# Performance work log

Measured on AMD Instinct MI355X. Metric: run time of the kernel, lower is better.

The kernel has to match this reference:

```python
import jax, jax.numpy as jnp
import numpy as np

B, H, W, C = 16, 32, 32, 512
L, CT = 77, 512
NH, HD = 8, 64
G = 32          # GroupNorm groups
EPS = 1e-6      # flax GroupNorm default epsilon
NEG = -1e10


def group_norm(x, scale, bias):
    # flax GroupNorm on [b, n, c]: stats over (n, channels-within-group) per (b, group)
    b, n, c = x.shape
    xg = x.reshape(b, n, G, c // G)
    mu = xg.mean(axis=(1, 3), keepdims=True)
    var = xg.var(axis=(1, 3), keepdims=True)
    xg = (xg - mu) * jax.lax.rsqrt(var + EPS)
    return xg.reshape(b, n, c) * scale + bias


def setup_inputs() -> dict:
    key = jax.random.key(0)
    ks = jax.random.split(key, 8)
    w = lambda k, shape: jax.random.normal(k, shape, jnp.float32) * 0.02
    return {
        "inputs": jax.random.normal(ks[0], (B, H, W, C), jnp.float32),
        "text_enc": jax.random.normal(ks[1], (B, L, CT), jnp.float32),
        "text_mask": jnp.ones((B, L), jnp.int32),
        "gn_q_scale": jnp.ones((C,), jnp.float32),
        "gn_q_bias": jnp.zeros((C,), jnp.float32),
        "gn_kv_scale": jnp.ones((C,), jnp.float32),
        "gn_kv_bias": jnp.zeros((C,), jnp.float32),
        "gn_t_scale": jnp.ones((CT,), jnp.float32),
        "gn_t_bias": jnp.zeros((CT,), jnp.float32),
        "Wq": w(ks[2], (C, NH, HD)),
        "Wk_self": w(ks[3], (C, NH, HD)),
        "Wv_self": w(ks[4], (C, NH, HD)),
        "Wk_cross": w(ks[5], (CT, NH, HD)),
        "Wv_cross": w(ks[6], (CT, NH, HD)),
        "Wout": w(ks[7], (NH, HD, C)),
    }


def reference(inputs, text_enc, text_mask,
              gn_q_scale, gn_q_bias, gn_kv_scale, gn_kv_bias,
              gn_t_scale, gn_t_bias,
              Wq, Wk_self, Wv_self, Wk_cross, Wv_cross, Wout):
    b, h, w, c = inputs.shape
    n = h * w
    x = inputs.reshape(b, n, c)

    x_q = group_norm(x, gn_q_scale, gn_q_bias)
    x_kv = group_norm(x, gn_kv_scale, gn_kv_bias)
    t = group_norm(text_enc, gn_t_scale, gn_t_bias)

    # q/k/v projections; fused: KV = concat(self-KV from image, cross-KV from text)
    scale = jnp.asarray(1.0 / np.sqrt(HD), inputs.dtype)
    q = jnp.einsum('bqc,chd->bqhd', x_q, Wq) * scale  # scale_attn_logits
    k = jnp.concatenate([jnp.einsum('bkc,chd->bkhd', x_kv, Wk_self),
                         jnp.einsum('blc,chd->blhd', t, Wk_cross)], axis=1)
    v = jnp.concatenate([jnp.einsum('bkc,chd->bkhd', x_kv, Wv_self),
                         jnp.einsum('blc,chd->blhd', t, Wv_cross)], axis=1)

    # make_attention_mask(ones[b,n], concat(ones[b,n], text_mask)) -> [b,1,n,n+l];
    # query mask is all ones so only the KV mask matters.
    kv_mask = jnp.concatenate(
        [jnp.ones((b, n), jnp.bool_), text_mask > 0], axis=1)  # [b, n+l]

    logits = jnp.einsum('bqhd,bkhd->bhqk', q, k)  # [b, nh, n, n+l]
    logits = jnp.where(kv_mask[:, None, None, :], logits, jnp.asarray(NEG, logits.dtype))
    probs = jax.nn.softmax(logits, axis=-1)
    attn = jnp.einsum('bhqk,bkhd->bqhd', probs, v)
    out = jnp.einsum('bqhd,hdc->bqc', attn, Wout)
    return out.reshape(b, h, w, c) + inputs
```

## Files before the change

kernel.cpp:

```cpp
#include <hip/hip_runtime.h>
#include <hip/hip_bf16.h>

typedef __hip_bfloat16 bf16;
typedef __attribute__((ext_vector_type(4))) short short4v;
typedef __attribute__((ext_vector_type(8))) short short8;
typedef __attribute__((ext_vector_type(4))) float f32x4;
typedef __attribute__((ext_vector_type(16))) float f32x16;
#define MFMA16(a, b, c) __builtin_amdgcn_mfma_f32_16x16x32_bf16(a, b, c, 0, 0, 0)
#define MFMA32(a, b, c) __builtin_amdgcn_mfma_f32_32x32x16_bf16(a, b, c, 0, 0, 0)

#define BB   16
#define CCH  512
#define NN   1024
#define LLT  77
#define LPAD 128
#define NHH  8
#define HDD  64
#define GGN  32
#define NKV  1101
#define KVP  1152

__device__ __forceinline__ unsigned short f2bu(float f){
  bf16 h = __float2bfloat16(f);
  return *reinterpret_cast<unsigned short*>(&h);
}

__device__ __forceinline__ unsigned pk2(float lo, float hi){
  __hip_bfloat162 h = __float22bfloat162_rn(make_float2(lo, hi));
  return *reinterpret_cast<unsigned*>(&h);
}

__device__ __forceinline__ void pl32swap(unsigned &a, unsigned &b){
  asm("v_permlane32_swap_b32 %0, %1" : "+v"(a), "+v"(b));
}

__global__ __launch_bounds__(256) void gn_stats_kernel(
    const float* __restrict__ ximg, const float* __restrict__ xtxt,
    float* __restrict__ stats )
{
  int isimg = blockIdx.x < 512;
  int bid = blockIdx.x & 511;
  int b = bid >> 5, g = bid & 31;
  int npos = isimg ? NN : LLT;
  const float* xb = (isimg ? ximg : xtxt) + (size_t)b * npos * CCH + g * 16;
  int tot4 = npos * 4;
  float s = 0.f, s2 = 0.f;
  for (int e = threadIdx.x; e < tot4; e += 256){
    int n = e >> 2, cq = (e & 3) * 4;
    float4 v = *(const float4*)(xb + (size_t)n * CCH + cq);
    s  += v.x + v.y + v.z + v.w;
    s2 += v.x * v.x + v.y * v.y + v.z * v.z + v.w * v.w;
  }
  __shared__ float sh1[256], sh2[256];
  sh1[threadIdx.x] = s; sh2[threadIdx.x] = s2;
  __syncthreads();
  for (int off = 128; off > 0; off >>= 1){
    if (threadIdx.x < off){
      sh1[threadIdx.x] += sh1[threadIdx.x + off];
      sh2[threadIdx.x] += sh2[threadIdx.x + off];
    }
    __syncthreads();
  }
  if (threadIdx.x == 0){
    float inv = 1.f / (float)(npos * 16);
    float m = sh1[0] * inv;
    float var = sh2[0] * inv - m * m;
    float* mu = stats + (isimg ? 0 : 1024);
    mu[bid] = m;
    mu[512 + bid] = rsqrtf(var + 1e-6f);
  }
}

__global__ __launch_bounds__(256) void prep_weights_kernel(
    const float* __restrict__ W0, const float* __restrict__ W1,
    const float* __restrict__ W2, const float* __restrict__ W3,
    const float* __restrict__ W4, const float* __restrict__ W5,
    bf16* __restrict__ Wt)
{
  int wsel = blockIdx.z;
  const float* W = wsel == 0 ? W0 : wsel == 1 ? W1 : wsel == 2 ? W2 :
                   wsel == 3 ? W3 : wsel == 4 ? W4 : W5;
  bf16* dst = Wt + (size_t)wsel * CCH * CCH;
  int n0 = blockIdx.x * 64, k0 = blockIdx.y * 64;

  __shared__ alignas(16) float Ws[64][68];
  int r = threadIdx.x >> 2, c = (threadIdx.x & 3) * 16;
  const float* src = W + (size_t)(k0 + r) * CCH + n0 + c;
  *(float4*)&Ws[r][c]      = *(const float4*)(src);
  *(float4*)&Ws[r][c + 4]  = *(const float4*)(src + 4);
  *(float4*)&Ws[r][c + 8]  = *(const float4*)(src + 8);
  *(float4*)&Ws[r][c + 12] = *(const float4*)(src + 12);
  __syncthreads();

  int nr = threadIdx.x >> 2, kc = (threadIdx.x & 3) * 16;
  union { uint4 v[2]; unsigned short s[16]; } o;
  #pragma unroll
  for (int j = 0; j < 16; j++) o.s[j] = f2bu(Ws[kc + j][nr]);
  bf16* d = dst + (size_t)(n0 + nr) * CCH + k0 + kc;
  *(uint4*)d = o.v[0];
  *(uint4*)(d + 8) = o.v[1];
}

__global__ __launch_bounds__(256) void norm_all_kernel(
    const float* __restrict__ x, const float* __restrict__ t,
    const float* __restrict__ stats,
    const float* __restrict__ gqs, const float* __restrict__ gqb,
    const float* __restrict__ gks, const float* __restrict__ gkb,
    const float* __restrict__ gts, const float* __restrict__ gtb,
    bf16* __restrict__ Xq, bf16* __restrict__ Xkv, bf16* __restrict__ Tn)
{
  if (blockIdx.x < 4096){
    size_t e = ((size_t)blockIdx.x * 256 + threadIdx.x) * 8;
    int b  = (int)(e >> 19);
    int ch = (int)(e & 511);
    int g  = ch >> 4;
    float m = stats[b * GGN + g], r = stats[512 + b * GGN + g];
    float4 x0 = *(const float4*)(x + e);
    float4 x1 = *(const float4*)(x + e + 4);
    float4 sq0 = *(const float4*)(gqs + ch), sq1 = *(const float4*)(gqs + ch + 4);
    float4 bq0 = *(const float4*)(gqb + ch), bq1 = *(const float4*)(gqb + ch + 4);
    float4 sk0 = *(const float4*)(gks + ch), sk1 = *(const float4*)(gks + ch + 4);
    float4 bk0 = *(const float4*)(gkb + ch), bk1 = *(const float4*)(gkb + ch + 4);
    float xs[8] = {x0.x,x0.y,x0.z,x0.w,x1.x,x1.y,x1.z,x1.w};
    float sqv[8] = {sq0.x,sq0.y,sq0.z,sq0.w,sq1.x,sq1.y,sq1.z,sq1.w};
    float bqv[8] = {bq0.x,bq0.y,bq0.z,bq0.w,bq1.x,bq1.y,bq1.z,bq1.w};
    float skv[8] = {sk0.x,sk0.y,sk0.z,sk0.w,sk1.x,sk1.y,sk1.z,sk1.w};
    float bkv[8] = {bk0.x,bk0.y,bk0.z,bk0.w,bk1.x,bk1.y,bk1.z,bk1.w};
    union { uint4 v; unsigned short s[8]; } oq, ok;
    #pragma unroll
    for (int j = 0; j < 8; j++){
      float nx = (xs[j] - m) * r;
      oq.s[j] = f2bu((nx * sqv[j] + bqv[j]) * 0.18033688f);
      ok.s[j] = f2bu(nx * skv[j] + bkv[j]);
    }
    *(uint4*)(Xq + e)  = oq.v;
    *(uint4*)(Xkv + e) = ok.v;
  } else {
    size_t e = ((size_t)(blockIdx.x - 4096) * 256 + threadIdx.x) * 8;
    int b  = (int)(e >> 16);
    int rem = (int)(e & 65535);
    int l  = rem >> 9;
    int ch = rem & 511;
    union { uint4 v; unsigned short s[8]; } o;
    if (l < LLT){
      int g = ch >> 4;
      float m = stats[1024 + b * GGN + g], r = stats[1536 + b * GGN + g];
      const float* src = t + ((size_t)b * LLT + l) * CCH + ch;
      float4 x0 = *(const float4*)src, x1 = *(const float4*)(src + 4);
      float4 s0 = *(const float4*)(gts + ch), s1 = *(const float4*)(gts + ch + 4);
      float4 b0 = *(const float4*)(gtb + ch), b1 = *(const float4*)(gtb + ch + 4);
      float xs[8] = {x0.x,x0.y,x0.z,x0.w,x1.x,x1.y,x1.z,x1.w};
      float sv[8] = {s0.x,s0.y,s0.z,s0.w,s1.x,s1.y,s1.z,s1.w};
      float bv[8] = {b0.x,b0.y,b0.z,b0.w,b1.x,b1.y,b1.z,b1.w};
      #pragma unroll
      for (int j = 0; j < 8; j++) o.s[j] = f2bu((xs[j] - m) * r * sv[j] + bv[j]);
    } else {
      o.v = make_uint4(0, 0, 0, 0);
    }
    *(uint4*)(Tn + e) = o.v;
  }
}

__global__ __launch_bounds__(256) void proj_self_mfma(
    const bf16* __restrict__ Xq, const bf16* __restrict__ Xkv,
    const bf16* __restrict__ Wt,
    bf16* __restrict__ Qo, bf16* __restrict__ Ko, bf16* __restrict__ Vo)
{
  const int tid  = threadIdx.x;
  const int wave = tid >> 6, lane = tid & 63;
  const int l16 = lane & 15, quad = lane >> 4;
  const int h  = blockIdx.x;
  const int n0 = blockIdx.y * 64;
  const int b  = blockIdx.z;

  __shared__ bf16 Aq[64][72], Ak[64][72];
  __shared__ bf16 Bq[64][72], Bk[64][72], Bv[64][72];

  const bf16* Wq  = Wt;
  const bf16* Wks = Wt + 1 * CCH * CCH;
  const bf16* Wvs = Wt + 2 * CCH * CCH;

  f32x4 sq[4], sk[4], sv[4];
  #pragma unroll
  for (int nt = 0; nt < 4; nt++){
    sq[nt] = (f32x4){0.f,0.f,0.f,0.f};
    sk[nt] = (f32x4){0.f,0.f,0.f,0.f};
    sv[nt] = (f32x4){0.f,0.f,0.f,0.f};
  }

  const int sr = tid >> 2, sc = (tid & 3) * 16;
  const bf16* p_aq = Xq  + ((size_t)b * NN + n0 + sr) * CCH + sc;
  const bf16* p_ak = Xkv + ((size_t)b * NN + n0 + sr) * CCH + sc;
  const bf16* p_bq = Wq  + (size_t)(h * 64 + sr) * CCH + sc;
  const bf16* p_bk = Wks + (size_t)(h * 64 + sr) * CCH + sc;
  const bf16* p_bv = Wvs + (size_t)(h * 64 + sr) * CCH + sc;

  uint4 raq0 = *(const uint4*)p_aq,       raq1 = *(const uint4*)(p_aq + 8);
  uint4 rak0 = *(const uint4*)p_ak,       rak1 = *(const uint4*)(p_ak + 8);
  uint4 rbq0 = *(const uint4*)p_bq,       rbq1 = *(const uint4*)(p_bq + 8);
  uint4 rbk0 = *(const uint4*)p_bk,       rbk1 = *(const uint4*)(p_bk + 8);
  uint4 rbv0 = *(const uint4*)p_bv,       rbv1 = *(const uint4*)(p_bv + 8);

  for (int kt = 0; kt < 8; kt++){
    *(uint4*)&Aq[sr][sc]     = raq0;  *(uint4*)&Aq[sr][sc + 8] = raq1;
    *(uint4*)&Ak[sr][sc]     = rak0;  *(uint4*)&Ak[sr][sc + 8] = rak1;
    *(uint4*)&Bq[sr][sc]     = rbq0;  *(uint4*)&Bq[sr][sc + 8] = rbq1;
    *(uint4*)&Bk[sr][sc]     = rbk0;  *(uint4*)&Bk[sr][sc + 8] = rbk1;
    *(uint4*)&Bv[sr][sc]     = rbv0;  *(uint4*)&Bv[sr][sc + 8] = rbv1;
    if (kt < 7){
      const int k1 = (kt + 1) * 64;
      raq0 = *(const uint4*)(p_aq + k1);  raq1 = *(const uint4*)(p_aq + k1 + 8);
      rak0 = *(const uint4*)(p_ak + k1);  rak1 = *(const uint4*)(p_ak + k1 + 8);
      rbq0 = *(const uint4*)(p_bq + k1);  rbq1 = *(const uint4*)(p_bq + k1 + 8);
      rbk0 = *(const uint4*)(p_bk + k1);  rbk1 = *(const uint4*)(p_bk + k1 + 8);
      rbv0 = *(const uint4*)(p_bv + k1);  rbv1 = *(const uint4*)(p_bv + k1 + 8);
    }
    __syncthreads();

    const short8 aq0 = *(const short8*)&Aq[wave * 16 + l16][quad * 8];
    const short8 aq1 = *(const short8*)&Aq[wave * 16 + l16][32 + quad * 8];
    const short8 ak0 = *(const short8*)&Ak[wave * 16 + l16][quad * 8];
    const short8 ak1 = *(const short8*)&Ak[wave * 16 + l16][32 + quad * 8];

    #pragma unroll
    for (int nt = 0; nt < 4; nt++){
      const short8 bq0 = *(const short8*)&Bq[nt * 16 + l16][quad * 8];
      const short8 bq1 = *(const short8*)&Bq[nt * 16 + l16][32 + quad * 8];
      sq[nt] = MFMA16(aq0, bq0, sq[nt]);
      sq[nt] = MFMA16(aq1, bq1, sq[nt]);
      const short8 bk0 = *(const short8*)&Bk[nt * 16 + l16][quad * 8];
      const short8 bk1 = *(const short8*)&Bk[nt * 16 + l16][32 + quad * 8];
      sk[nt] = MFMA16(ak0, bk0, sk[nt]);
      sk[nt] = MFMA16(ak1, bk1, sk[nt]);
      const short8 bv0 = *(const short8*)&Bv[nt * 16 + l16][quad * 8];
      const short8 bv1 = *(const short8*)&Bv[nt * 16 + l16][32 + quad * 8];
      sv[nt] = MFMA16(ak0, bv0, sv[nt]);
      sv[nt] = MFMA16(ak1, bv1, sv[nt]);
    }
    __syncthreads();
  }

  #pragma unroll
  for (int r = 0; r < 4; r++){
    int n = n0 + wave * 16 + quad * 4 + r;
    bf16* qd = Qo + (((size_t)b * NHH + h) * NN + n) * HDD + l16;
    bf16* kd = Ko + (((size_t)b * NHH + h) * KVP + n) * HDD + l16;
    #pragma unroll
    for (int nt = 0; nt < 4; nt++){
      qd[nt * 16] = __float2bfloat16(sq[nt][r]);
      kd[nt * 16] = __float2bfloat16(sk[nt][r]);
    }
  }

  __syncthreads();
  #pragma unroll
  for (int nt = 0; nt < 4; nt++)
    #pragma unroll
    for (int r = 0; r < 4; r++)
      Bq[nt * 16 + l16][wave * 16 + quad * 4 + r] = __float2bfloat16(sv[nt][r]);
  __syncthreads();
  {
    int d = tid >> 2, c = (tid & 3) * 16;
    bf16* vd = Vo + (((size_t)b * NHH + h) * HDD + d) * KVP + n0 + c;
    *(uint4*)vd       = *(const uint4*)&Bq[d][c];
    *(uint4*)(vd + 8) = *(const uint4*)&Bq[d][c + 8];
  }
}

__global__ __launch_bounds__(256) void proj_cross_mfma(
    const bf16* __restrict__ Tn, const bf16* __restrict__ Wt,
    bf16* __restrict__ Ko, bf16* __restrict__ Vo)
{
  const int tid  = threadIdx.x;
  const int wave = tid >> 6, lane = tid & 63;
  const int l16 = lane & 15, quad = lane >> 4;
  const int h  = blockIdx.x;
  const int l0 = blockIdx.y * 64;
  const int b  = blockIdx.z;

  __shared__ bf16 At[64][72];
  __shared__ bf16 Bk[64][72], Bv[64][72];

  const bf16* Wkc = Wt + 3 * CCH * CCH;
  const bf16* Wvc = Wt + 4 * CCH * CCH;

  f32x4 sk[4], sv[4];
  #pragma unroll
  for (int nt = 0; nt < 4; nt++){
    sk[nt] = (f32x4){0.f,0.f,0.f,0.f};
    sv[nt] = (f32x4){0.f,0.f,0.f,0.f};
  }

  const int sr = tid >> 2, sc = (tid & 3) * 16;
  const bf16* p_a  = Tn  + ((size_t)b * LPAD + l0 + sr) * CCH + sc;
  const bf16* p_bk = Wkc + (size_t)(h * 64 + sr) * CCH + sc;
  const bf16* p_bv = Wvc + (size_t)(h * 64 + sr) * CCH + sc;

  uint4 ra0 = *(const uint4*)p_a,   ra1 = *(const uint4*)(p_a + 8);
  uint4 rk0 = *(const uint4*)p_bk,  rk1 = *(const uint4*)(p_bk + 8);
  uint4 rv0 = *(const uint4*)p_bv,  rv1 = *(const uint4*)(p_bv + 8);

  for (int kt = 0; kt < 8; kt++){
    *(uint4*)&At[sr][sc]     = ra0;  *(uint4*)&At[sr][sc + 8] = ra1;
    *(uint4*)&Bk[sr][sc]     = rk0;  *(uint4*)&Bk[sr][sc + 8] = rk1;
    *(uint4*)&Bv[sr][sc]     = rv0;  *(uint4*)&Bv[sr][sc + 8] = rv1;
    if (kt < 7){
      const int k1 = (kt + 1) * 64;
      ra0 = *(const uint4*)(p_a + k1);   ra1 = *(const uint4*)(p_a + k1 + 8);
      rk0 = *(const uint4*)(p_bk + k1);  rk1 = *(const uint4*)(p_bk + k1 + 8);
      rv0 = *(const uint4*)(p_bv + k1);  rv1 = *(const uint4*)(p_bv + k1 + 8);
    }
    __syncthreads();

    const short8 a0 = *(const short8*)&At[wave * 16 + l16][quad * 8];
    const short8 a1 = *(const short8*)&At[wave * 16 + l16][32 + quad * 8];
    #pragma unroll
    for (int nt = 0; nt < 4; nt++){
      const short8 bk0 = *(const short8*)&Bk[nt * 16 + l16][quad * 8];
      const short8 bk1 = *(const short8*)&Bk[nt * 16 + l16][32 + quad * 8];
      sk[nt] = MFMA16(a0, bk0, sk[nt]);
      sk[nt] = MFMA16(a1, bk1, sk[nt]);
      const short8 bv0 = *(const short8*)&Bv[nt * 16 + l16][quad * 8];
      const short8 bv1 = *(const short8*)&Bv[nt * 16 + l16][32 + quad * 8];
      sv[nt] = MFMA16(a0, bv0, sv[nt]);
      sv[nt] = MFMA16(a1, bv1, sv[nt]);
    }
    __syncthreads();
  }

  #pragma unroll
  for (int r = 0; r < 4; r++){
    int kvrow = NN + l0 + wave * 16 + quad * 4 + r;
    bf16* kd = Ko + (((size_t)b * NHH + h) * KVP + kvrow) * HDD + l16;
    #pragma unroll
    for (int nt = 0; nt < 4; nt++)
      kd[nt * 16] = __float2bfloat16(sk[nt][r]);
  }

  __syncthreads();
  #pragma unroll
  for (int nt = 0; nt < 4; nt++)
    #pragma unroll
    for (int r = 0; r < 4; r++)
      Bk[nt * 16 + l16][wave * 16 + quad * 4 + r] = __float2bfloat16(sv[nt][r]);
  __syncthreads();
  {
    int d = tid >> 2, c = (tid & 3) * 16;
    bf16* vd = Vo + (((size_t)b * NHH + h) * HDD + d) * KVP + NN + l0 + c;
    *(uint4*)vd       = *(const uint4*)&Bk[d][c];
    *(uint4*)(vd + 8) = *(const uint4*)&Bk[d][c + 8];
  }
}

__global__ __launch_bounds__(256, 4) void attn_mfma_kernel(
    const bf16* __restrict__ Q, const bf16* __restrict__ K,
    const bf16* __restrict__ Vt, const int* __restrict__ tmask,
    bf16* __restrict__ Ao)
{
  const int tid  = threadIdx.x;
  const int wave = tid >> 6;
  const int lane = tid & 63;
  const int l31  = lane & 31;
  const int hi   = lane >> 5;
  const int q0 = blockIdx.x * 128;
  const int h  = blockIdx.y;
  const int b  = blockIdx.z;

  __shared__ alignas(16) bf16 KV[2][2][64][72];

  const bf16* qp = Q + (((size_t)b * NHH + h) * NN + q0 + wave * 32 + l31) * HDD + hi * 8;
  short8 qf[4];
  qf[0] = *(const short8*)(qp);
  qf[1] = *(const short8*)(qp + 16);
  qf[2] = *(const short8*)(qp + 32);
  qf[3] = *(const short8*)(qp + 48);

  f32x16 o_acc[2];
  #pragma unroll
  for (int dt = 0; dt < 2; dt++)
    #pragma unroll
    for (int i = 0; i < 16; i++) o_acc[dt][i] = 0.f;
  float lrow = 0.f;

  const size_t kbase = ((size_t)b * NHH + h) * KVP;
  const size_t vbase = ((size_t)b * NHH + h) * (size_t)HDD * KVP;

  const int sr = tid >> 2;
  const int sc = (tid & 3) * 16;
  const bf16* kp = K  + (kbase + sr) * HDD + sc;
  const bf16* vp = Vt + vbase + (size_t)sr * KVP + sc;

  uint4 kr0 = *(const uint4*)kp, kr1 = *(const uint4*)(kp + 8);
  uint4 vr0 = *(const uint4*)vp, vr1 = *(const uint4*)(vp + 8);
  *(uint4*)&KV[0][0][sr][sc]     = kr0;
  *(uint4*)&KV[0][0][sr][sc + 8] = kr1;
  *(uint4*)&KV[0][1][sr][sc]     = vr0;
  *(uint4*)&KV[0][1][sr][sc + 8] = vr1;
  kr0 = *(const uint4*)(kp + 4096); kr1 = *(const uint4*)(kp + 4096 + 8);
  vr0 = *(const uint4*)(vp + 64);   vr1 = *(const uint4*)(vp + 64 + 8);
  __syncthreads();

  for (int kt = 0; kt < 18; kt++){
    const int cur = kt & 1;
    if (kt + 1 < 18){
      *(uint4*)&KV[cur ^ 1][0][sr][sc]     = kr0;
      *(uint4*)&KV[cur ^ 1][0][sr][sc + 8] = kr1;
      *(uint4*)&KV[cur ^ 1][1][sr][sc]     = vr0;
      *(uint4*)&KV[cur ^ 1][1][sr][sc + 8] = vr1;
    }
    if (kt + 2 < 18){
      const size_t ko = (size_t)(kt + 2) * 4096;
      const int    vo = (kt + 2) * 64;
      kr0 = *(const uint4*)(kp + ko); kr1 = *(const uint4*)(kp + ko + 8);
      vr0 = *(const uint4*)(vp + vo); vr1 = *(const uint4*)(vp + vo + 8);
    }

    const bf16 (*Ks)[72] = KV[cur][0];
    const bf16 (*Vs)[72] = KV[cur][1];
    const int kv0 = kt * 64;

    #pragma unroll
    for (int t = 0; t < 2; t++){
      f32x16 s;
      #pragma unroll
      for (int i = 0; i < 16; i++) s[i] = 0.f;
      const short8 kf0 = *(const short8*)&Ks[t * 32 + l31][hi * 8];
      const short8 kf1 = *(const short8*)&Ks[t * 32 + l31][16 + hi * 8];
      const short8 kf2 = *(const short8*)&Ks[t * 32 + l31][32 + hi * 8];
      const short8 kf3 = *(const short8*)&Ks[t * 32 + l31][48 + hi * 8];
      s = MFMA32(kf0, qf[0], s);
      s = MFMA32(kf1, qf[1], s);
      s = MFMA32(kf2, qf[2], s);
      s = MFMA32(kf3, qf[3], s);

      if (kv0 + 64 > NN){
        #pragma unroll
        for (int r = 0; r < 16; r++){
          int idx = kv0 - NN + t * 32 + (r & 3) + 8 * (r >> 2) + 4 * hi;
          int ci = idx < LLT ? idx : LLT - 1;
          float rep = (idx < LLT)
                        ? (tmask[b * LLT + ci] > 0 ? 1e30f : -1e10f)
                        : -1e30f;
          s[r] = fminf(s[r], rep);
        }
      }

      #pragma unroll
      for (int r = 0; r < 16; r++){
        s[r] = exp2f(s[r]);
        lrow += s[r];
      }

      unsigned w0 = pk2(s[0],  s[1]),  w1 = pk2(s[2],  s[3]);
      unsigned w2 = pk2(s[4],  s[5]),  w3 = pk2(s[6],  s[7]);
      unsigned w4 = pk2(s[8],  s[9]),  w5 = pk2(s[10], s[11]);
      unsigned w6 = pk2(s[12], s[13]), w7 = pk2(s[14], s[15]);
      pl32swap(w0, w2);
      pl32swap(w1, w3);
      pl32swap(w4, w6);
      pl32swap(w5, w7);
      union { unsigned u[4]; short8 s8; } pf0, pf1;
      pf0.u[0] = w0; pf0.u[1] = w1; pf0.u[2] = w2; pf0.u[3] = w3;
      pf1.u[0] = w4; pf1.u[1] = w5; pf1.u[2] = w6; pf1.u[3] = w7;

      #pragma unroll
      for (int dt = 0; dt < 2; dt++){
        const short8 vf0 = *(const short8*)&Vs[dt * 32 + l31][t * 32 + hi * 8];
        const short8 vf1 = *(const short8*)&Vs[dt * 32 + l31][t * 32 + 16 + hi * 8];
        o_acc[dt] = MFMA32(pf0.s8, vf0, o_acc[dt]);
        o_acc[dt] = MFMA32(pf1.s8, vf1, o_acc[dt]);
      }
    }
    __syncthreads();
  }

  lrow += __shfl_xor(lrow, 32);
  #pragma unroll
  for (int r = 0; r < 16; r++){
    const int ql = (r & 3) + 8 * (r >> 2) + 4 * hi;
    float linv = 1.f / __shfl(lrow, ql);
    const int n = q0 + wave * 32 + ql;
    bf16* dst = Ao + ((size_t)b * NN + n) * CCH + h * HDD + l31;
    dst[0]  = __float2bfloat16(o_acc[0][r] * linv);
    dst[32] = __float2bfloat16(o_acc[1][r] * linv);
  }
}

__global__ __launch_bounds__(256) void outproj_mfma(
    const bf16* __restrict__ A, const bf16* __restrict__ Wt,
    const float* __restrict__ resid, float* __restrict__ out)
{
  const int tid  = threadIdx.x;
  const int wave = tid >> 6, lane = tid & 63;
  const int l16 = lane & 15, quad = lane >> 4;
  const int col0 = blockIdx.x * 64;
  const int n0   = blockIdx.y * 64;
  const int b    = blockIdx.z;

  __shared__ bf16 As[64][72], Bs[64][72];
  const bf16* Wo = Wt + 5 * CCH * CCH;

  f32x4 o[4];
  #pragma unroll
  for (int nt = 0; nt < 4; nt++) o[nt] = (f32x4){0.f,0.f,0.f,0.f};

  const int sr = tid >> 2, sc = (tid & 3) * 16;
  const bf16* p_a = A  + ((size_t)b * NN + n0 + sr) * CCH + sc;
  const bf16* p_b = Wo + (size_t)(col0 + sr) * CCH + sc;

  uint4 ra0 = *(const uint4*)p_a,  ra1 = *(const uint4*)(p_a + 8);
  uint4 rb0 = *(const uint4*)p_b,  rb1 = *(const uint4*)(p_b + 8);

  for (int kt = 0; kt < 8; kt++){
    *(uint4*)&As[sr][sc]     = ra0;  *(uint4*)&As[sr][sc + 8] = ra1;
    *(uint4*)&Bs[sr][sc]     = rb0;  *(uint4*)&Bs[sr][sc + 8] = rb1;
    if (kt < 7){
      const int k1 = (kt + 1) * 64;
      ra0 = *(const uint4*)(p_a + k1);  ra1 = *(const uint4*)(p_a + k1 + 8);
      rb0 = *(const uint4*)(p_b + k1);  rb1 = *(const uint4*)(p_b + k1 + 8);
    }
    __syncthreads();

    const short8 a0 = *(const short8*)&As[wave * 16 + l16][quad * 8];
    const short8 a1 = *(const short8*)&As[wave * 16 + l16][32 + quad * 8];
    #pragma unroll
    for (int nt = 0; nt < 4; nt++){
      const short8 b0 = *(const short8*)&Bs[nt * 16 + l16][quad * 8];
      const short8 b1 = *(const short8*)&Bs[nt * 16 + l16][32 + quad * 8];
      o[nt] = MFMA16(a0, b0, o[nt]);
      o[nt] = MFMA16(a1, b1, o[nt]);
    }
    __syncthreads();
  }

  #pragma unroll
  for (int r = 0; r < 4; r++){
    size_t row = (size_t)b * NN + n0 + wave * 16 + quad * 4 + r;
    #pragma unroll
    for (int nt = 0; nt < 4; nt++){
      int col = col0 + nt * 16 + l16;
      out[row * CCH + col] = o[nt][r] + resid[row * CCH + col];
    }
  }
}

extern "C" void kernel_launch(void* const* d_in, const int* in_sizes, int n_in,
                              void* d_out, int out_size, void* d_ws, size_t ws_size,
                              hipStream_t stream)
{
  const float* x     = (const float*)d_in[0];
  const float* txt   = (const float*)d_in[1];
  const int*   tmask = (const int*)d_in[2];
  const float* gqs   = (const float*)d_in[3];
  const float* gqb   = (const float*)d_in[4];
  const float* gks   = (const float*)d_in[5];
  const float* gkb   = (const float*)d_in[6];
  const float* gts   = (const float*)d_in[7];
  const float* gtb   = (const float*)d_in[8];
  const float* Wq    = (const float*)d_in[9];
  const float* Wks   = (const float*)d_in[10];
  const float* Wvs   = (const float*)d_in[11];
  const float* Wkc   = (const float*)d_in[12];
  const float* Wvc   = (const float*)d_in[13];
  const float* Wout  = (const float*)d_in[14];

  float* stats = (float*)d_ws;
  bf16* WtAll = (bf16*)(stats + 2048);
  bf16* Xq  = WtAll + (size_t)6 * CCH * CCH;
  bf16* Xkv = Xq  + (size_t)BB * NN * CCH;
  bf16* Tn  = Xkv + (size_t)BB * NN * CCH;
  bf16* Qw  = Tn  + (size_t)BB * LPAD * CCH;
  bf16* Kw  = Qw  + (size_t)BB * NHH * NN * HDD;
  bf16* Vw  = Kw  + (size_t)BB * NHH * KVP * HDD;
  bf16* Aw  = Xq;

  gn_stats_kernel<<<1024, 256, 0, stream>>>(x, txt, stats);
  prep_weights_kernel<<<dim3(8, 8, 6), 256, 0, stream>>>(
      Wq, Wks, Wvs, Wkc, Wvc, Wout, WtAll);
  norm_all_kernel<<<4608, 256, 0, stream>>>(
      x, txt, stats, gqs, gqb, gks, gkb, gts, gtb, Xq, Xkv, Tn);
  proj_self_mfma<<<dim3(8, 16, BB), 256, 0, stream>>>(
      Xq, Xkv, WtAll, Qw, Kw, Vw);
  proj_cross_mfma<<<dim3(8, 2, BB), 256, 0, stream>>>(
      Tn, WtAll, Kw, Vw);
  attn_mfma_kernel<<<dim3(8, NHH, BB), 256, 0, stream>>>(Qw, Kw, Vw, tmask, Aw);
  outproj_mfma<<<dim3(8, 16, BB), 256, 0, stream>>>(Aw, WtAll, x, (float*)d_out);
}
```

Baseline: 288.9 us.

## Use 128x128 block tiles for projection GEMMs and MFMA row-sum in attention

```diff
diff --git a/kernel.cpp b/kernel.cpp
--- a/kernel.cpp
+++ b/kernel.cpp
@@ -2,7 +2,6 @@
 #include <hip/hip_bf16.h>
 
 typedef __hip_bfloat16 bf16;
-typedef __attribute__((ext_vector_type(4))) short short4v;
 typedef __attribute__((ext_vector_type(8))) short short8;
 typedef __attribute__((ext_vector_type(4))) float f32x4;
 typedef __attribute__((ext_vector_type(16))) float f32x16;
@@ -169,101 +168,106 @@
   const int tid  = threadIdx.x;
   const int wave = tid >> 6, lane = tid & 63;
   const int l16 = lane & 15, quad = lane >> 4;
-  const int h  = blockIdx.x;
-  const int n0 = blockIdx.y * 64;
-  const int b  = blockIdx.z;
-
-  __shared__ bf16 Aq[64][72], Ak[64][72];
-  __shared__ bf16 Bq[64][72], Bk[64][72], Bv[64][72];
-
-  const bf16* Wq  = Wt;
-  const bf16* Wks = Wt + 1 * CCH * CCH;
-  const bf16* Wvs = Wt + 2 * CCH * CCH;
-
-  f32x4 sq[4], sk[4], sv[4];
-  #pragma unroll
-  for (int nt = 0; nt < 4; nt++){
-    sq[nt] = (f32x4){0.f,0.f,0.f,0.f};
-    sk[nt] = (f32x4){0.f,0.f,0.f,0.f};
-    sv[nt] = (f32x4){0.f,0.f,0.f,0.f};
-  }
+  const int wr = wave >> 1, wc = wave & 1;
+  const int ct = blockIdx.x;
+  const int rt = blockIdx.y;
+  const int mat = ct >> 2;
+  const int cm0 = (ct & 3) * 128;
+  const int b  = rt >> 3;
+  const int n0 = (rt & 7) * 128;
+
+  __shared__ bf16 T[4][64][72];
+
+  const bf16* A  = (mat == 0) ? Xq : Xkv;
+  const bf16* Bw = Wt + (size_t)mat * CCH * CCH + (size_t)cm0 * CCH;
+
+  f32x4 acc[4][4];
+  #pragma unroll
+  for (int rf = 0; rf < 4; rf++)
+    #pragma unroll
+    for (int cf = 0; cf < 4; cf++) acc[rf][cf] = (f32x4){0.f,0.f,0.f,0.f};
 
   const int sr = tid >> 2, sc = (tid & 3) * 16;
-  const bf16* p_aq = Xq  + ((size_t)b * NN + n0 + sr) * CCH + sc;
-  const bf16* p_ak = Xkv + ((size_t)b * NN + n0 + sr) * CCH + sc;
-  const bf16* p_bq = Wq  + (size_t)(h * 64 + sr) * CCH + sc;
-  const bf16* p_bk = Wks + (size_t)(h * 64 + sr) * CCH + sc;
-  const bf16* p_bv = Wvs + (size_t)(h * 64 + sr) * CCH + sc;
-
-  uint4 raq0 = *(const uint4*)p_aq,       raq1 = *(const uint4*)(p_aq + 8);
-  uint4 rak0 = *(const uint4*)p_ak,       rak1 = *(const uint4*)(p_ak + 8);
-  uint4 rbq0 = *(const uint4*)p_bq,       rbq1 = *(const uint4*)(p_bq + 8);
-  uint4 rbk0 = *(const uint4*)p_bk,       rbk1 = *(const uint4*)(p_bk + 8);
-  uint4 rbv0 = *(const uint4*)p_bv,       rbv1 = *(const uint4*)(p_bv + 8);
+  const bf16* pa0 = A  + ((size_t)b * NN + n0 + sr) * CCH + sc;
+  const bf16* pa1 = pa0 + (size_t)64 * CCH;
+  const bf16* pb0 = Bw + (size_t)sr * CCH + sc;
+  const bf16* pb1 = pb0 + (size_t)64 * CCH;
+
+  uint4 rA0a = *(const uint4*)pa0, rA0b = *(const uint4*)(pa0 + 8);
+  uint4 rA1a = *(const uint4*)pa1, rA1b = *(const uint4*)(pa1 + 8);
+  uint4 rB0a = *(const uint4*)pb0, rB0b = *(const uint4*)(pb0 + 8);
+  uint4 rB1a = *(const uint4*)pb1, rB1b = *(const uint4*)(pb1 + 8);
 
   for (int kt = 0; kt < 8; kt++){
-    *(uint4*)&Aq[sr][sc]     = raq0;  *(uint4*)&Aq[sr][sc + 8] = raq1;
-    *(uint4*)&Ak[sr][sc]     = rak0;  *(uint4*)&Ak[sr][sc + 8] = rak1;
-    *(uint4*)&Bq[sr][sc]     = rbq0;  *(uint4*)&Bq[sr][sc + 8] = rbq1;
-    *(uint4*)&Bk[sr][sc]     = rbk0;  *(uint4*)&Bk[sr][sc + 8] = rbk1;
-    *(uint4*)&Bv[sr][sc]     = rbv0;  *(uint4*)&Bv[sr][sc + 8] = rbv1;
+    *(uint4*)&T[0][sr][sc] = rA0a;  *(uint4*)&T[0][sr][sc + 8] = rA0b;
+    *(uint4*)&T[1][sr][sc] = rA1a;  *(uint4*)&T[1][sr][sc + 8] = rA1b;
+    *(uint4*)&T[2][sr][sc] = rB0a;  *(uint4*)&T[2][sr][sc + 8] = rB0b;
+    *(uint4*)&T[3][sr][sc] = rB1a;  *(uint4*)&T[3][sr][sc + 8] = rB1b;
     if (kt < 7){
       const int k1 = (kt + 1) * 64;
-      raq0 = *(const uint4*)(p_aq + k1);  raq1 = *(const uint4*)(p_aq + k1 + 8);
-      rak0 = *(const uint4*)(p_ak + k1);  rak1 = *(const uint4*)(p_ak + k1 + 8);
-      rbq0 = *(const uint4*)(p_bq + k1);  rbq1 = *(const uint4*)(p_bq + k1 + 8);
-      rbk0 = *(const uint4*)(p_bk + k1);  rbk1 = *(const uint4*)(p_bk + k1 + 8);
-      rbv0 = *(const uint4*)(p_bv + k1);  rbv1 = *(const uint4*)(p_bv + k1 + 8);
-    }
-    __syncthreads();
-
-    const short8 aq0 = *(const short8*)&Aq[wave * 16 + l16][quad * 8];
-    const short8 aq1 = *(const short8*)&Aq[wave * 16 + l16][32 + quad * 8];
-    const short8 ak0 = *(const short8*)&Ak[wave * 16 + l16][quad * 8];
-    const short8 ak1 = *(const short8*)&Ak[wave * 16 + l16][32 + quad * 8];
-
-    #pragma unroll
-    for (int nt = 0; nt < 4; nt++){
-      const short8 bq0 = *(const short8*)&Bq[nt * 16 + l16][quad * 8];
-      const short8 bq1 = *(const short8*)&Bq[nt * 16 + l16][32 + quad * 8];
-      sq[nt] = MFMA16(aq0, bq0, sq[nt]);
-      sq[nt] = MFMA16(aq1, bq1, sq[nt]);
-      const short8 bk0 = *(const short8*)&Bk[nt * 16 + l16][quad * 8];
-      const short8 bk1 = *(const short8*)&Bk[nt * 16 + l16][32 + quad * 8];
-      sk[nt] = MFMA16(ak0, bk0, sk[nt]);
-      sk[nt] = MFMA16(ak1, bk1, sk[nt]);
-      const short8 bv0 = *(const short8*)&Bv[nt * 16 + l16][quad * 8];
-      const short8 bv1 = *(const short8*)&Bv[nt * 16 + l16][32 + quad * 8];
-      sv[nt] = MFMA16(ak0, bv0, sv[nt]);
-      sv[nt] = MFMA16(ak1, bv1, sv[nt]);
-    }
-    __syncthreads();
-  }
-
-  #pragma unroll
-  for (int r = 0; r < 4; r++){
-    int n = n0 + wave * 16 + quad * 4 + r;
-    bf16* qd = Qo + (((size_t)b * NHH + h) * NN + n) * HDD + l16;
-    bf16* kd = Ko + (((size_t)b * NHH + h) * KVP + n) * HDD + l16;
-    #pragma unroll
-    for (int nt = 0; nt < 4; nt++){
-      qd[nt * 16] = __float2bfloat16(sq[nt][r]);
-      kd[nt * 16] = __float2bfloat16(sk[nt][r]);
-    }
-  }
-
-  __syncthreads();
-  #pragma unroll
-  for (int nt = 0; nt < 4; nt++)
-    #pragma unroll
-    for (int r = 0; r < 4; r++)
-      Bq[nt * 16 + l16][wave * 16 + quad * 4 + r] = __float2bfloat16(sv[nt][r]);
-  __syncthreads();
-  {
-    int d = tid >> 2, c = (tid & 3) * 16;
-    bf16* vd = Vo + (((size_t)b * NHH + h) * HDD + d) * KVP + n0 + c;
-    *(uint4*)vd       = *(const uint4*)&Bq[d][c];
-    *(uint4*)(vd + 8) = *(const uint4*)&Bq[d][c + 8];
+      rA0a = *(const uint4*)(pa0 + k1);  rA0b = *(const uint4*)(pa0 + k1 + 8);
+      rA1a = *(const uint4*)(pa1 + k1);  rA1b = *(const uint4*)(pa1 + k1 + 8);
+      rB0a = *(const uint4*)(pb0 + k1);  rB0b = *(const uint4*)(pb0 + k1 + 8);
+      rB1a = *(const uint4*)(pb1 + k1);  rB1b = *(const uint4*)(pb1 + k1 + 8);
+    }
+    __syncthreads();
+
+    short8 af[4][2];
+    #pragma unroll
+    for (int rf = 0; rf < 4; rf++){
+      af[rf][0] = *(const short8*)&T[wr][rf * 16 + l16][quad * 8];
+      af[rf][1] = *(const short8*)&T[wr][rf * 16 + l16][32 + quad * 8];
+    }
+    #pragma unroll
+    for (int cf = 0; cf < 4; cf++){
+      const short8 b0 = *(const short8*)&T[2 + wc][cf * 16 + l16][quad * 8];
+      const short8 b1 = *(const short8*)&T[2 + wc][cf * 16 + l16][32 + quad * 8];
+      #pragma unroll
+      for (int rf = 0; rf < 4; rf++){
+        acc[rf][cf] = MFMA16(af[rf][0], b0, acc[rf][cf]);
+        acc[rf][cf] = MFMA16(af[rf][1], b1, acc[rf][cf]);
+      }
+    }
+    __syncthreads();
+  }
+
+  if (mat < 2){
+    bf16* Out = (mat == 0) ? Qo : Ko;
+    const int stride = (mat == 0) ? NN : KVP;
+    #pragma unroll
+    for (int cf = 0; cf < 4; cf++){
+      const int cm = cm0 + wc * 64 + cf * 16 + l16;
+      const int h = cm >> 6, d = cm & 63;
+      #pragma unroll
+      for (int rf = 0; rf < 4; rf++)
+        #pragma unroll
+        for (int r = 0; r < 4; r++){
+          const int n = n0 + wr * 64 + rf * 16 + quad * 4 + r;
+          Out[(((size_t)b * NHH + h) * stride + n) * HDD + d] =
+              __float2bfloat16(acc[rf][cf][r]);
+        }
+    }
+  } else {
+    bf16 (*Tw)[72] = T[wave];
+    #pragma unroll
+    for (int cf = 0; cf < 4; cf++)
+      #pragma unroll
+      for (int rf = 0; rf < 4; rf++)
+        #pragma unroll
+        for (int r = 0; r < 4; r++)
+          Tw[cf * 16 + l16][rf * 16 + quad * 4 + r] =
+              __float2bfloat16(acc[rf][cf][r]);
+    __syncthreads();
+    const int h  = (cm0 + wc * 64) >> 6;
+    const int nb = n0 + wr * 64;
+    const int dl = lane >> 2, cseg = (lane & 3) * 16;
+    #pragma unroll
+    for (int k2 = 0; k2 < 4; k2++){
+      const int d = dl + k2 * 16;
+      bf16* vd = Vo + (((size_t)b * NHH + h) * HDD + d) * KVP + nb + cseg;
+      *(uint4*)vd       = *(const uint4*)&Tw[d][cseg];
+      *(uint4*)(vd + 8) = *(const uint4*)&Tw[d][cseg + 8];
+    }
   }
 }
 
@@ -375,12 +379,21 @@
   qf[2] = *(const short8*)(qp + 32);
   qf[3] = *(const short8*)(qp + 48);
 
-  f32x16 o_acc[2];
+  union { unsigned u[4]; short8 s8; } ones;
+  ones.u[0] = 0x3F803F80u; ones.u[1] = 0x3F803F80u;
+  ones.u[2] = 0x3F803F80u; ones.u[3] = 0x3F803F80u;
+
+  f32x16 zf;
+  #pragma unroll
+  for (int i = 0; i < 16; i++) zf[i] = 0.f;
+
+  f32x16 o_acc[2], l_acc;
   #pragma unroll
   for (int dt = 0; dt < 2; dt++)
     #pragma unroll
     for (int i = 0; i < 16; i++) o_acc[dt][i] = 0.f;
-  float lrow = 0.f;
+  #pragma unroll
+  for (int i = 0; i < 16; i++) l_acc[i] = 0.f;
 
   const size_t kbase = ((size_t)b * NHH + h) * KVP;
   const size_t vbase = ((size_t)b * NHH + h) * (size_t)HDD * KVP;
@@ -421,14 +434,11 @@
 
     #pragma unroll
     for (int t = 0; t < 2; t++){
-      f32x16 s;
-      #pragma unroll
-      for (int i = 0; i < 16; i++) s[i] = 0.f;
       const short8 kf0 = *(const short8*)&Ks[t * 32 + l31][hi * 8];
       const short8 kf1 = *(const short8*)&Ks[t * 32 + l31][16 + hi * 8];
       const short8 kf2 = *(const short8*)&Ks[t * 32 + l31][32 + hi * 8];
       const short8 kf3 = *(const short8*)&Ks[t * 32 + l31][48 + hi * 8];
-      s = MFMA32(kf0, qf[0], s);
+      f32x16 s = MFMA32(kf0, qf[0], zf);
       s = MFMA32(kf1, qf[1], s);
       s = MFMA32(kf2, qf[2], s);
       s = MFMA32(kf3, qf[3], s);
@@ -446,10 +456,7 @@
       }
 
       #pragma unroll
-      for (int r = 0; r < 16; r++){
-        s[r] = exp2f(s[r]);
-        lrow += s[r];
-      }
+      for (int r = 0; r < 16; r++) s[r] = exp2f(s[r]);
 
       unsigned w0 = pk2(s[0],  s[1]),  w1 = pk2(s[2],  s[3]);
       unsigned w2 = pk2(s[4],  s[5]),  w3 = pk2(s[6],  s[7]);
@@ -463,6 +470,9 @@
       pf0.u[0] = w0; pf0.u[1] = w1; pf0.u[2] = w2; pf0.u[3] = w3;
       pf1.u[0] = w4; pf1.u[1] = w5; pf1.u[2] = w6; pf1.u[3] = w7;
 
+      l_acc = MFMA32(pf0.s8, ones.s8, l_acc);
+      l_acc = MFMA32(pf1.s8, ones.s8, l_acc);
+
       #pragma unroll
       for (int dt = 0; dt < 2; dt++){
         const short8 vf0 = *(const short8*)&Vs[dt * 32 + l31][t * 32 + hi * 8];
@@ -474,11 +484,10 @@
     __syncthreads();
   }
 
-  lrow += __shfl_xor(lrow, 32);
   #pragma unroll
   for (int r = 0; r < 16; r++){
     const int ql = (r & 3) + 8 * (r >> 2) + 4 * hi;
-    float linv = 1.f / __shfl(lrow, ql);
+    const float linv = 1.f / l_acc[r];
     const int n = q0 + wave * 32 + ql;
     bf16* dst = Ao + ((size_t)b * NN + n) * CCH + h * HDD + l31;
     dst[0]  = __float2bfloat16(o_acc[0][r] * linv);
@@ -493,55 +502,74 @@
   const int tid  = threadIdx.x;
   const int wave = tid >> 6, lane = tid & 63;
   const int l16 = lane & 15, quad = lane >> 4;
-  const int col0 = blockIdx.x * 64;
-  const int n0   = blockIdx.y * 64;
-  const int b    = blockIdx.z;
-
-  __shared__ bf16 As[64][72], Bs[64][72];
-  const bf16* Wo = Wt + 5 * CCH * CCH;
-
-  f32x4 o[4];
-  #pragma unroll
-  for (int nt = 0; nt < 4; nt++) o[nt] = (f32x4){0.f,0.f,0.f,0.f};
+  const int wr = wave >> 1, wc = wave & 1;
+  const int c0 = blockIdx.x * 128;
+  const int g0 = blockIdx.y * 128;
+
+  __shared__ bf16 T[4][64][72];
+  const bf16* Bw = Wt + (size_t)5 * CCH * CCH + (size_t)c0 * CCH;
+
+  f32x4 acc[4][4];
+  #pragma unroll
+  for (int rf = 0; rf < 4; rf++)
+    #pragma unroll
+    for (int cf = 0; cf < 4; cf++) acc[rf][cf] = (f32x4){0.f,0.f,0.f,0.f};
 
   const int sr = tid >> 2, sc = (tid & 3) * 16;
-  const bf16* p_a = A  + ((size_t)b * NN + n0 + sr) * CCH + sc;
-  const bf16* p_b = Wo + (size_t)(col0 + sr) * CCH + sc;
-
-  uint4 ra0 = *(const uint4*)p_a,  ra1 = *(const uint4*)(p_a + 8);
-  uint4 rb0 = *(const uint4*)p_b,  rb1 = *(const uint4*)(p_b + 8);
+  const bf16* pa0 = A  + ((size_t)g0 + sr) * CCH + sc;
+  const bf16* pa1 = pa0 + (size_t)64 * CCH;
+  const bf16* pb0 = Bw + (size_t)sr * CCH + sc;
+  const bf16* pb1 = pb0 + (size_t)64 * CCH;
+
+  uint4 rA0a = *(const uint4*)pa0, rA0b = *(const uint4*)(pa0 + 8);
+  uint4 rA1a = *(const uint4*)pa1, rA1b = *(const uint4*)(pa1 + 8);
+  uint4 rB0a = *(const uint4*)pb0, rB0b = *(const uint4*)(pb0 + 8);
+  uint4 rB1a = *(const uint4*)pb1, rB1b = *(const uint4*)(pb1 + 8);
 
   for (int kt = 0; kt < 8; kt++){
-    *(uint4*)&As[sr][sc]     = ra0;  *(uint4*)&As[sr][sc + 8] = ra1;
-    *(uint4*)&Bs[sr][sc]     = rb0;  *(uint4*)&Bs[sr][sc + 8] = rb1;
+    *(uint4*)&T[0][sr][sc] = rA0a;  *(uint4*)&T[0][sr][sc + 8] = rA0b;
+    *(uint4*)&T[1][sr][sc] = rA1a;  *(uint4*)&T[1][sr][sc + 8] = rA1b;
+    *(uint4*)&T[2][sr][sc] = rB0a;  *(uint4*)&T[2][sr][sc + 8] = rB0b;
+    *(uint4*)&T[3][sr][sc] = rB1a;  *(uint4*)&T[3][sr][sc + 8] = rB1b;
     if (kt < 7){
       const int k1 = (kt + 1) * 64;
-      ra0 = *(const uint4*)(p_a + k1);  ra1 = *(const uint4*)(p_a + k1 + 8);
-      rb0 = *(const uint4*)(p_b + k1);  rb1 = *(const uint4*)(p_b + k1 + 8);
-    }
-    __syncthreads();
-
-    const short8 a0 = *(const short8*)&As[wave * 16 + l16][quad * 8];
-    const short8 a1 = *(const short8*)&As[wave * 16 + l16][32 + quad * 8];
-    #pragma unroll
-    for (int nt = 0; nt < 4; nt++){
-      const short8 b0 = *(const short8*)&Bs[nt * 16 + l16][quad * 8];
-      const short8 b1 = *(const short8*)&Bs[nt * 16 + l16][32 + quad * 8];
-      o[nt] = MFMA16(a0, b0, o[nt]);
-      o[nt] = MFMA16(a1, b1, o[nt]);
-    }
-    __syncthreads();
-  }
-
-  #pragma unroll
-  for (int r = 0; r < 4; r++){
-    size_t row = (size_t)b * NN + n0 + wave * 16 + quad * 4 + r;
-    #pragma unroll
-    for (int nt = 0; nt < 4; nt++){
-      int col = col0 + nt * 16 + l16;
-      out[row * CCH + col] = o[nt][r] + resid[row * CCH + col];
-    }
-  }
+      rA0a = *(const uint4*)(pa0 + k1);  rA0b = *(const uint4*)(pa0 + k1 + 8);
+      rA1a = *(const uint4*)(pa1 + k1);  rA1b = *(const uint4*)(pa1 + k1 + 8);
+      rB0a = *(const uint4*)(pb0 + k1);  rB0b = *(const uint4*)(pb0 + k1 + 8);
+      rB1a = *(const uint4*)(pb1 + k1);  rB1b = *(const uint4*)(pb1 + k1 + 8);
+    }
+    __syncthreads();
+
+    short8 af[4][2];
+    #pragma unroll
+    for (int rf = 0; rf < 4; rf++){
+      af[rf][0] = *(const short8*)&T[wr][rf * 16 + l16][quad * 8];
+      af[rf][1] = *(const short8*)&T[wr][rf * 16 + l16][32 + quad * 8];
+    }
+    #pragma unroll
+    for (int cf = 0; cf < 4; cf++){
+      const short8 b0 = *(const short8*)&T[2 + wc][cf * 16 + l16][quad * 8];
+      const short8 b1 = *(const short8*)&T[2 + wc][cf * 16 + l16][32 + quad * 8];
+      #pragma unroll
+      for (int rf = 0; rf < 4; rf++){
+        acc[rf][cf] = MFMA16(af[rf][0], b0, acc[rf][cf]);
+        acc[rf][cf] = MFMA16(af[rf][1], b1, acc[rf][cf]);
+      }
+    }
+    __syncthreads();
+  }
+
+  #pragma unroll
+  for (int rf = 0; rf < 4; rf++)
+    #pragma unroll
+    for (int r = 0; r < 4; r++){
+      const size_t row = (size_t)g0 + wr * 64 + rf * 16 + quad * 4 + r;
+      #pragma unroll
+      for (int cf = 0; cf < 4; cf++){
+        const int col = c0 + wc * 64 + cf * 16 + l16;
+        out[row * CCH + col] = acc[rf][cf][r] + resid[row * CCH + col];
+      }
+    }
 }
 
 extern "C" void kernel_launch(void* const* d_in, const int* in_sizes, int n_in,
@@ -579,10 +607,10 @@
       Wq, Wks, Wvs, Wkc, Wvc, Wout, WtAll);
   norm_all_kernel<<<4608, 256, 0, stream>>>(
       x, txt, stats, gqs, gqb, gks, gkb, gts, gtb, Xq, Xkv, Tn);
-  proj_self_mfma<<<dim3(8, 16, BB), 256, 0, stream>>>(
+  proj_self_mfma<<<dim3(12, 128), 256, 0, stream>>>(
       Xq, Xkv, WtAll, Qw, Kw, Vw);
   proj_cross_mfma<<<dim3(8, 2, BB), 256, 0, stream>>>(
       Tn, WtAll, Kw, Vw);
   attn_mfma_kernel<<<dim3(8, NHH, BB), 256, 0, stream>>>(Qw, Kw, Vw, tmask, Aw);
-  outproj_mfma<<<dim3(8, 16, BB), 256, 0, stream>>>(Aw, WtAll, x, (float*)d_out);
-}
+  outproj_mfma<<<dim3(4, 128), 256, 0, stream>>>(Aw, WtAll, x, (float*)d_out);
+}
```

After: 277.7 us. 1.04x faster.
